# Kernel tuning notes

Measured on AMD Instinct MI355X. Metric: run time of the kernel, lower is better.

Reference implementation:

```python
import jax, jax.numpy as jnp
import numpy as np
import math

EMB_DIM = 1024
HEADS = 16
HEAD_DIM = EMB_DIM // HEADS
B, S = 2, 2048


def setup_inputs() -> dict:
    key = jax.random.key(0)
    k1, k2, k3, k4, k5 = jax.random.split(key, 5)
    X = jax.random.normal(k1, (B, S, EMB_DIM), dtype=jnp.float32)
    # causal mask: positions with 0.0 are masked to -inf (masked_fill(mask == 0.0, -inf))
    mask = jnp.tril(jnp.ones((S, S), dtype=jnp.float32))
    scale = 1.0 / math.sqrt(EMB_DIM)
    # torch Linear(emb_dim, 3*emb_dim): y = x @ W.T + b; store W pre-transposed [E, 3E]
    W_qkv = jax.random.normal(k2, (EMB_DIM, 3 * EMB_DIM), dtype=jnp.float32) * scale
    b_qkv = jnp.zeros((3 * EMB_DIM,), dtype=jnp.float32)
    W_o = jax.random.normal(k3, (EMB_DIM, EMB_DIM), dtype=jnp.float32) * scale
    b_o = jnp.zeros((EMB_DIM,), dtype=jnp.float32)
    return {"X": X, "mask": mask, "W_qkv": W_qkv, "b_qkv": b_qkv, "W_o": W_o, "b_o": b_o}


def reference(X, mask, W_qkv, b_qkv, W_o, b_o):
    # X: [B, S, E]
    Bn, Sn, E = X.shape
    qkv = X @ W_qkv + b_qkv                                   # [B, S, 3E]
    qkv = qkv.reshape(Bn, Sn, 3, HEADS, HEAD_DIM)
    qkv = jnp.transpose(qkv, (2, 0, 3, 1, 4))                  # [3, B, H, S, d]
    Q, K, V = qkv[0], qkv[1], qkv[2]
    inv_sqrt_d = 1.0 / math.sqrt(HEAD_DIM)
    scores = jnp.einsum('bhqd,bhkd->bhqk', Q, K) * inv_sqrt_d  # [B, H, S, S]
    scores = jnp.where(mask == 0.0, -jnp.inf, scores)
    attn = jax.nn.softmax(scores, axis=-1)
    # dropout omitted (eval mode / deterministic reference)
    out = jnp.einsum('bhqk,bhkd->bhqd', attn, V)               # [B, H, S, d]
    out = jnp.transpose(out, (0, 2, 1, 3)).reshape(Bn, Sn, E)
    return out @ W_o + b_o
```

## Files before the change

### kernel.cpp

```cpp
#include <hip/hip_runtime.h>
#include <hip/hip_bf16.h>
#include <cstdint>
#include <cstddef>

typedef __bf16 bf16_t;
typedef __attribute__((ext_vector_type(8))) __bf16 bf16x8;
typedef __attribute__((ext_vector_type(4))) __bf16 bf16x4;
typedef __attribute__((ext_vector_type(4))) float f32x4;

#define AS1 __attribute__((address_space(1)))
#define AS3 __attribute__((address_space(3)))

static constexpr int Bn = 2, Sn = 2048, En = 1024, Hn = 16, Dn = 64;

__device__ __forceinline__ uint32_t cvt_pk_bf16(float lo, float hi) {
  uint32_t r;
  asm("v_cvt_pk_bf16_f32 %0, %1, %2" : "=v"(r) : "v"(lo), "v"(hi));
  return r;
}

__global__ __launch_bounds__(256) void convert_f32_bf16(
    const float* __restrict__ in, bf16_t* __restrict__ out, int n) {
  int i = (blockIdx.x * 256 + threadIdx.x) * 4;
  if (i < n) {
    float4 v = *(const float4*)(in + i);
    bf16x4 o;
    o[0] = (bf16_t)v.x; o[1] = (bf16_t)v.y; o[2] = (bf16_t)v.z; o[3] = (bf16_t)v.w;
    *(bf16x4*)(out + i) = o;
  }
}

__global__ __launch_bounds__(256) void transpose_conv(
    const float* __restrict__ in, bf16_t* __restrict__ out, int R, int C) {
  __shared__ float tile[32][33];
  int bx = blockIdx.x * 32, by = blockIdx.y * 32;
  int tx = threadIdx.x & 31, ty = threadIdx.x >> 5;
#pragma unroll
  for (int i = 0; i < 32; i += 8)
    tile[ty + i][tx] = in[(size_t)(by + ty + i) * C + bx + tx];
  __syncthreads();
#pragma unroll
  for (int i = 0; i < 32; i += 8)
    out[(size_t)(bx + ty + i) * R + by + tx] = (bf16_t)tile[tx][ty + i];
}

__global__ __launch_bounds__(256) void transpose_v(
    const bf16_t* __restrict__ V, bf16_t* __restrict__ Vt) {
  __shared__ ushort tile[64][65];
  int bh = blockIdx.y, s0 = blockIdx.x * 64;
  int t = threadIdx.x;
  const ushort* src = (const ushort*)(V + ((size_t)bh * Sn + s0) * 64);
#pragma unroll
  for (int p = 0; p < 4; ++p) {
    int s = p * 16 + (t >> 4);
    int c = (t & 15) * 4;
    ushort4 v = *(const ushort4*)(src + (size_t)s * 64 + c);
    tile[s][c] = v.x; tile[s][c + 1] = v.y; tile[s][c + 2] = v.z; tile[s][c + 3] = v.w;
  }
  __syncthreads();
  ushort* dst = (ushort*)(Vt + ((size_t)bh * 64) * Sn + s0);
#pragma unroll
  for (int p = 0; p < 4; ++p) {
    int d = p * 16 + (t >> 4);
    int c = (t & 15) * 4;
    ushort4 v;
    v.x = tile[c][d]; v.y = tile[c + 1][d]; v.z = tile[c + 2][d]; v.w = tile[c + 3][d];
    *(ushort4*)(dst + (size_t)d * Sn + c) = v;
  }
}

template <int K_>
__device__ __forceinline__ void gemm_core(
    const bf16_t* __restrict__ A, const bf16_t* __restrict__ Bt,
    f32x4 (&acc)[4][4], int& col0, int& row0) {
  __shared__ bf16_t As[2][128 * 32];
  __shared__ bf16_t Bs[2][128 * 32];
  const int tid = threadIdx.x, lane = tid & 63, wid = tid >> 6;
  const int wm = wid >> 1, wn = wid & 1;
  const int m0 = blockIdx.y * 128, n0 = blockIdx.x * 128;
  const int KT = K_ / 32;

  auto stage = [&](bf16_t* as, bf16_t* bs, int kt) {
    int csw = ((lane & 3) ^ ((lane >> 2) & 3)) * 8;
#pragma unroll
    for (int j = 0; j < 2; ++j) {
      int r0 = wid * 32 + j * 16;
      const bf16_t* ga = A + (size_t)(m0 + r0 + (lane >> 2)) * K_ + kt * 32 + csw;
      __builtin_amdgcn_global_load_lds((const AS1 void*)ga, (AS3 void*)(as + r0 * 32), 16, 0, 0);
      const bf16_t* gb = Bt + (size_t)(n0 + r0 + (lane >> 2)) * K_ + kt * 32 + csw;
      __builtin_amdgcn_global_load_lds((const AS1 void*)gb, (AS3 void*)(bs + r0 * 32), 16, 0, 0);
    }
  };
  auto compute = [&](const bf16_t* as, const bf16_t* bs) {
    bf16x8 af[4], bfr[4];
    uint32_t swz = (uint32_t)(((lane >> 4) ^ (lane & 3)) << 4);
#pragma unroll
    for (int mi = 0; mi < 4; ++mi) {
      uint32_t row = (uint32_t)(wm * 64 + mi * 16 + (lane & 15));
      af[mi] = *(const bf16x8*)((const char*)as + row * 64 + swz);
    }
#pragma unroll
    for (int ni = 0; ni < 4; ++ni) {
      uint32_t row = (uint32_t)(wn * 64 + ni * 16 + (lane & 15));
      bfr[ni] = *(const bf16x8*)((const char*)bs + row * 64 + swz);
    }
#pragma unroll
    for (int mi = 0; mi < 4; ++mi)
#pragma unroll
      for (int ni = 0; ni < 4; ++ni)
        acc[mi][ni] = __builtin_amdgcn_mfma_f32_16x16x32_bf16(af[mi], bfr[ni], acc[mi][ni], 0, 0, 0);
  };

  stage(As[0], Bs[0], 0);
  __syncthreads();
  int cur = 0;
  for (int kt = 0; kt < KT - 1; ++kt) {
    stage(As[cur ^ 1], Bs[cur ^ 1], kt + 1);
    compute(As[cur], Bs[cur]);
    __syncthreads();
    cur ^= 1;
  }
  compute(As[cur], Bs[cur]);
  col0 = n0 + wn * 64 + (lane & 15);
  row0 = m0 + wm * 64 + ((lane >> 4) << 2);
}

__global__ __launch_bounds__(256) void gemm_qkv(
    const bf16_t* __restrict__ A, const bf16_t* __restrict__ Bt,
    const float* __restrict__ bias, bf16_t* __restrict__ Qb,
    bf16_t* __restrict__ Kb, bf16_t* __restrict__ Vb) {
  f32x4 acc[4][4] = {};
  int col0, row0;
  gemm_core<1024>(A, Bt, acc, col0, row0);
#pragma unroll
  for (int ni = 0; ni < 4; ++ni) {
    int n = col0 + ni * 16;
    float bv = bias[n];
    int which = n >> 10, nn = n & 1023;
    int h = nn >> 6, dd = nn & 63;
    bf16_t* dst = which == 0 ? Qb : (which == 1 ? Kb : Vb);
    float scl = which == 0 ? 0.125f * 1.44269504f : 1.0f;
#pragma unroll
    for (int mi = 0; mi < 4; ++mi)
#pragma unroll
      for (int i = 0; i < 4; ++i) {
        int m = row0 + mi * 16 + i;
        int b = m >> 11, s = m & 2047;
        float v = (acc[mi][ni][i] + bv) * scl;
        dst[(((size_t)b * Hn + h) * Sn + s) * 64 + dd] = (bf16_t)v;
      }
  }
}

__global__ __launch_bounds__(256) void gemm_out(
    const bf16_t* __restrict__ A, const bf16_t* __restrict__ Bt,
    const float* __restrict__ bias, float* __restrict__ out) {
  f32x4 acc[4][4] = {};
  int col0, row0;
  gemm_core<1024>(A, Bt, acc, col0, row0);
#pragma unroll
  for (int ni = 0; ni < 4; ++ni) {
    int n = col0 + ni * 16;
    float bv = bias[n];
#pragma unroll
    for (int mi = 0; mi < 4; ++mi)
#pragma unroll
      for (int i = 0; i < 4; ++i) {
        int m = row0 + mi * 16 + i;
        out[(size_t)m * En + n] = acc[mi][ni][i] + bv;
      }
  }
}

__global__ __launch_bounds__(256) void attn_fwd(
    const bf16_t* __restrict__ Qb, const bf16_t* __restrict__ Kb,
    const bf16_t* __restrict__ Vt, bf16_t* __restrict__ AO) {
  __shared__ bf16_t Ks[2][64 * 64];
  __shared__ bf16_t Vs[2][64 * 64];
  __shared__ bf16_t Ps[4][16 * 64];
  const int tid = threadIdx.x, lane = tid & 63, wid = tid >> 6;
  const int bh = blockIdx.x;
  const int pr = blockIdx.y;

  const int rl = lane >> 3;
  const int cp = lane & 7;
  auto issueKV = [&](int buf, int t) {
#pragma unroll
    for (int j = 0; j < 2; ++j) {
      int r = wid * 16 + j * 8 + rl;
      int sc = cp ^ rl;
      const bf16_t* gk = Kb + (((size_t)bh * Sn + t * 64 + r) << 6) + (sc << 3);
      __builtin_amdgcn_global_load_lds((const AS1 void*)gk,
          (AS3 void*)(&Ks[buf][wid * 1024 + j * 512]), 16, 0, 0);
      const bf16_t* gv = Vt + ((size_t)bh * 64 + r) * Sn + t * 64 + (sc << 3);
      __builtin_amdgcn_global_load_lds((const AS1 void*)gv,
          (AS3 void*)(&Vs[buf][wid * 1024 + j * 512]), 16, 0, 0);
    }
  };

  const int srcA = (((lane & 15) + ((lane & 16) << 1)) << 2);
  const int srcB = srcA + 64;
  const bool hi = lane >= 32;

  int buf = 0;
  issueKV(0, 0);

  for (int seg = 0; seg < 2; ++seg) {
    const int q_tile = seg ? 31 - pr : pr;
    const int ntseg = q_tile + 1;
    const int qb = q_tile * 64 + wid * 16;
    const int qmy = qb + (lane & 15);

    bf16x8 aq[2];
    {
      const bf16_t* qp = Qb + ((size_t)bh * Sn + qb + (lane & 15)) * 64 + ((lane >> 4) << 3);
      aq[0] = *(const bf16x8*)qp;
      aq[1] = *(const bf16x8*)(qp + 32);
    }
    f32x4 O[4] = {};
    float m_run = -1e30f, l_run = 0.f;

    for (int t = 0; t < ntseg; ++t) {
      asm volatile("s_waitcnt vmcnt(0)" ::: "memory");
      __syncthreads();
      if (t + 1 < ntseg) issueKV(buf ^ 1, t + 1);
      else if (seg == 0) issueKV(buf ^ 1, 0);
      const char* ksb = (const char*)Ks[buf];
      const char* vsb = (const char*)Vs[buf];
      f32x4 sc[4];
      __builtin_amdgcn_s_setprio(1);
#pragma unroll
      for (int ni = 0; ni < 4; ++ni) {
        int kvr = ni * 16 + (lane & 15);
        uint32_t o0 = (uint32_t)(kvr * 128 + ((lane >> 4) << 4)) ^ (uint32_t)((kvr & 7) << 4);
        uint32_t o1 = (uint32_t)(kvr * 128 + 64 + ((lane >> 4) << 4)) ^ (uint32_t)((kvr & 7) << 4);
        bf16x8 b0 = *(const bf16x8*)(ksb + o0);
        bf16x8 b1 = *(const bf16x8*)(ksb + o1);
        f32x4 z = {};
        z = __builtin_amdgcn_mfma_f32_16x16x32_bf16(b0, aq[0], z, 0, 0, 0);
        sc[ni] = __builtin_amdgcn_mfma_f32_16x16x32_bf16(b1, aq[1], z, 0, 0, 0);
      }
      __builtin_amdgcn_s_setprio(0);
      if (t == ntseg - 1) {
#pragma unroll
        for (int ni = 0; ni < 4; ++ni) {
          int kvbase = t * 64 + ni * 16 + ((lane >> 4) << 2);
#pragma unroll
          for (int i = 0; i < 4; ++i)
            if (kvbase + i > qmy) sc[ni][i] = -1e30f;
        }
      }
      float mt = sc[0][0];
#pragma unroll
      for (int ni = 0; ni < 4; ++ni)
#pragma unroll
        for (int i = 0; i < 4; ++i) mt = fmaxf(mt, sc[ni][i]);
      mt = fmaxf(mt, __shfl_xor(mt, 16));
      mt = fmaxf(mt, __shfl_xor(mt, 32));
      if (!__all(mt <= m_run + 11.5f)) {
        float mn = fmaxf(m_run, mt);
        float s = __builtin_exp2f(m_run - mn);
        m_run = mn;
        l_run *= s;
#pragma unroll
        for (int n2 = 0; n2 < 4; ++n2)
#pragma unroll
          for (int i = 0; i < 4; ++i) O[n2][i] *= s;
      }
      float rs = 0.f;
      uint32_t pk[4][2];
#pragma unroll
      for (int ni = 0; ni < 4; ++ni) {
        float p0 = __builtin_exp2f(sc[ni][0] - m_run);
        float p1 = __builtin_exp2f(sc[ni][1] - m_run);
        float p2 = __builtin_exp2f(sc[ni][2] - m_run);
        float p3 = __builtin_exp2f(sc[ni][3] - m_run);
        rs += (p0 + p1) + (p2 + p3);
        pk[ni][0] = cvt_pk_bf16(p0, p1);
        pk[ni][1] = cvt_pk_bf16(p2, p3);
      }
      rs += __shfl_xor(rs, 16);
      rs += __shfl_xor(rs, 32);
      l_run += rs;
      union U8 { uint32_t u[4]; bf16x8 v; } pw0, pw1;
#pragma unroll
      for (int w = 0; w < 4; ++w) {
        int srci = (w < 2) ? srcA : srcB;
        uint32_t x0 = (uint32_t)__builtin_amdgcn_ds_bpermute(srci, (int)pk[0][w & 1]);
        uint32_t y0 = (uint32_t)__builtin_amdgcn_ds_bpermute(srci, (int)pk[1][w & 1]);
        pw0.u[w] = hi ? y0 : x0;
        uint32_t x1 = (uint32_t)__builtin_amdgcn_ds_bpermute(srci, (int)pk[2][w & 1]);
        uint32_t y1 = (uint32_t)__builtin_amdgcn_ds_bpermute(srci, (int)pk[3][w & 1]);
        pw1.u[w] = hi ? y1 : x1;
      }
      __builtin_amdgcn_s_setprio(1);
#pragma unroll
      for (int n2 = 0; n2 < 4; ++n2) {
        int dr = n2 * 16 + (lane & 15);
        uint32_t o0 = (uint32_t)(dr * 128 + ((lane >> 4) << 4)) ^ (uint32_t)((dr & 7) << 4);
        uint32_t o1 = (uint32_t)(dr * 128 + 64 + ((lane >> 4) << 4)) ^ (uint32_t)((dr & 7) << 4);
        bf16x8 v0 = *(const bf16x8*)(vsb + o0);
        bf16x8 v1 = *(const bf16x8*)(vsb + o1);
        O[n2] = __builtin_amdgcn_mfma_f32_16x16x32_bf16(v0, pw0.v, O[n2], 0, 0, 0);
        O[n2] = __builtin_amdgcn_mfma_f32_16x16x32_bf16(v1, pw1.v, O[n2], 0, 0, 0);
      }
      __builtin_amdgcn_s_setprio(0);
      buf ^= 1;
    }
    char* pw = (char*)Ps[wid];
    const float inv = 1.0f / l_run;
    const int ql = lane & 15, g = lane >> 4;
#pragma unroll
    for (int n2 = 0; n2 < 4; ++n2)
#pragma unroll
      for (int p2 = 0; p2 < 2; ++p2) {
        uint32_t w = cvt_pk_bf16(O[n2][2 * p2] * inv, O[n2][2 * p2 + 1] * inv);
        uint32_t byte = (uint32_t)(ql * 128 + n2 * 32 + g * 8 + p2 * 4) ^ (uint32_t)((ql & 7) << 4);
        *(uint32_t*)(pw + byte) = w;
      }
    asm volatile("s_waitcnt lgkmcnt(0)" ::: "memory");
    __builtin_amdgcn_sched_barrier(0);
    int b = bh >> 4, h = bh & 15;
#pragma unroll
    for (int i = 0; i < 4; ++i) {
      int ql2 = (g << 2) + i;
      int qrow = qb + ql2;
#pragma unroll
      for (int n2 = 0; n2 < 4; ++n2) {
        int d = n2 * 16 + ql;
        uint32_t byte = (uint32_t)(ql2 * 128 + d * 2) ^ (uint32_t)((ql2 & 7) << 4);
        AO[((size_t)b * Sn + qrow) * En + h * 64 + d] = *(bf16_t*)(pw + byte);
      }
    }
  }
}

extern "C" void kernel_launch(void* const* d_in, const int* in_sizes, int n_in,
                              void* d_out, int out_size, void* d_ws, size_t ws_size,
                              hipStream_t stream) {
  const float* X     = (const float*)d_in[0];
  const float* W_qkv = (const float*)d_in[2];
  const float* b_qkv = (const float*)d_in[3];
  const float* W_o   = (const float*)d_in[4];
  const float* b_o   = (const float*)d_in[5];
  float* out = (float*)d_out;

  char* ws = (char*)d_ws;
  bf16_t* Xb  = (bf16_t*)(ws);
  bf16_t* WqT = (bf16_t*)(ws + 8388608);
  bf16_t* WoT = (bf16_t*)(ws + 14680064);
  bf16_t* Qb  = (bf16_t*)(ws + 16777216);
  bf16_t* Kb  = (bf16_t*)(ws + 25165824);
  bf16_t* Vb  = (bf16_t*)(ws + 33554432);
  bf16_t* Vt  = (bf16_t*)(ws + 41943040);
  bf16_t* AO  = (bf16_t*)(ws + 50331648);

  convert_f32_bf16<<<4096, 256, 0, stream>>>(X, Xb, Bn * Sn * En);
  transpose_conv<<<dim3(96, 32), 256, 0, stream>>>(W_qkv, WqT, 1024, 3072);
  transpose_conv<<<dim3(32, 32), 256, 0, stream>>>(W_o, WoT, 1024, 1024);
  gemm_qkv<<<dim3(24, 32), 256, 0, stream>>>(Xb, WqT, b_qkv, Qb, Kb, Vb);
  transpose_v<<<dim3(32, 32), 256, 0, stream>>>(Vb, Vt);
  attn_fwd<<<dim3(32, 16), 256, 0, stream>>>(Qb, Kb, Vt, AO);
  gemm_out<<<dim3(8, 32), 256, 0, stream>>>(AO, WoT, b_o, out);
}
```

Baseline: 224.4 us.

## Split attention blocks to one query tile each and halve out-GEMM M tile

The attention kernel drops the paired-query-tile scheme, where each block handled tiles pr and 31-pr in sequence, and launches one block per query tile (grid 32x32). Blocks are ordered so the heaviest causal tiles come first. The output projection GEMM is templated to a 64-row M tile, which doubles its block count from 256 to 512 so it fills the GPU better. In exchange, the attention blocks now carry uneven amounts of work and the Q/O setup and write-back cost is paid per block, while the GEMM reuses the B tile over fewer rows.

```diff
diff --git a/kernel.cpp b/kernel.cpp
--- a/kernel.cpp
+++ b/kernel.cpp
@@ -69,34 +69,39 @@
   }
 }
 
-template <int K_>
+template <int K_, int BM>
 __device__ __forceinline__ void gemm_core(
     const bf16_t* __restrict__ A, const bf16_t* __restrict__ Bt,
-    f32x4 (&acc)[4][4], int& col0, int& row0) {
-  __shared__ bf16_t As[2][128 * 32];
+    f32x4 (&acc)[BM / 32][4], int& col0, int& row0) {
+  __shared__ bf16_t As[2][BM * 32];
   __shared__ bf16_t Bs[2][128 * 32];
   const int tid = threadIdx.x, lane = tid & 63, wid = tid >> 6;
   const int wm = wid >> 1, wn = wid & 1;
-  const int m0 = blockIdx.y * 128, n0 = blockIdx.x * 128;
+  const int m0 = blockIdx.y * BM, n0 = blockIdx.x * 128;
   const int KT = K_ / 32;
+  constexpr int MI = BM / 32;
 
   auto stage = [&](bf16_t* as, bf16_t* bs, int kt) {
     int csw = ((lane & 3) ^ ((lane >> 2) & 3)) * 8;
 #pragma unroll
+    for (int j = 0; j < BM / 64; ++j) {
+      int r0 = wid * (BM / 4) + j * 16;
+      const bf16_t* ga = A + (size_t)(m0 + r0 + (lane >> 2)) * K_ + kt * 32 + csw;
+      __builtin_amdgcn_global_load_lds((const AS1 void*)ga, (AS3 void*)(as + r0 * 32), 16, 0, 0);
+    }
+#pragma unroll
     for (int j = 0; j < 2; ++j) {
       int r0 = wid * 32 + j * 16;
-      const bf16_t* ga = A + (size_t)(m0 + r0 + (lane >> 2)) * K_ + kt * 32 + csw;
-      __builtin_amdgcn_global_load_lds((const AS1 void*)ga, (AS3 void*)(as + r0 * 32), 16, 0, 0);
       const bf16_t* gb = Bt + (size_t)(n0 + r0 + (lane >> 2)) * K_ + kt * 32 + csw;
       __builtin_amdgcn_global_load_lds((const AS1 void*)gb, (AS3 void*)(bs + r0 * 32), 16, 0, 0);
     }
   };
   auto compute = [&](const bf16_t* as, const bf16_t* bs) {
-    bf16x8 af[4], bfr[4];
+    bf16x8 af[MI], bfr[4];
     uint32_t swz = (uint32_t)(((lane >> 4) ^ (lane & 3)) << 4);
 #pragma unroll
-    for (int mi = 0; mi < 4; ++mi) {
-      uint32_t row = (uint32_t)(wm * 64 + mi * 16 + (lane & 15));
+    for (int mi = 0; mi < MI; ++mi) {
+      uint32_t row = (uint32_t)(wm * (BM / 2) + mi * 16 + (lane & 15));
       af[mi] = *(const bf16x8*)((const char*)as + row * 64 + swz);
     }
 #pragma unroll
@@ -105,7 +110,7 @@
       bfr[ni] = *(const bf16x8*)((const char*)bs + row * 64 + swz);
     }
 #pragma unroll
-    for (int mi = 0; mi < 4; ++mi)
+    for (int mi = 0; mi < MI; ++mi)
 #pragma unroll
       for (int ni = 0; ni < 4; ++ni)
         acc[mi][ni] = __builtin_amdgcn_mfma_f32_16x16x32_bf16(af[mi], bfr[ni], acc[mi][ni], 0, 0, 0);
@@ -122,7 +127,7 @@
   }
   compute(As[cur], Bs[cur]);
   col0 = n0 + wn * 64 + (lane & 15);
-  row0 = m0 + wm * 64 + ((lane >> 4) << 2);
+  row0 = m0 + wm * (BM / 2) + ((lane >> 4) << 2);
 }
 
 __global__ __launch_bounds__(256) void gemm_qkv(
@@ -131,7 +136,7 @@
     bf16_t* __restrict__ Kb, bf16_t* __restrict__ Vb) {
   f32x4 acc[4][4] = {};
   int col0, row0;
-  gemm_core<1024>(A, Bt, acc, col0, row0);
+  gemm_core<1024, 128>(A, Bt, acc, col0, row0);
 #pragma unroll
   for (int ni = 0; ni < 4; ++ni) {
     int n = col0 + ni * 16;
@@ -155,15 +160,15 @@
 __global__ __launch_bounds__(256) void gemm_out(
     const bf16_t* __restrict__ A, const bf16_t* __restrict__ Bt,
     const float* __restrict__ bias, float* __restrict__ out) {
-  f32x4 acc[4][4] = {};
+  f32x4 acc[2][4] = {};
   int col0, row0;
-  gemm_core<1024>(A, Bt, acc, col0, row0);
+  gemm_core<1024, 64>(A, Bt, acc, col0, row0);
 #pragma unroll
   for (int ni = 0; ni < 4; ++ni) {
     int n = col0 + ni * 16;
     float bv = bias[n];
 #pragma unroll
-    for (int mi = 0; mi < 4; ++mi)
+    for (int mi = 0; mi < 2; ++mi)
 #pragma unroll
       for (int i = 0; i < 4; ++i) {
         int m = row0 + mi * 16 + i;
@@ -180,7 +185,11 @@
   __shared__ bf16_t Ps[4][16 * 64];
   const int tid = threadIdx.x, lane = tid & 63, wid = tid >> 6;
   const int bh = blockIdx.x;
-  const int pr = blockIdx.y;
+  const int y = blockIdx.y, gy = y & 7, ky = y >> 3;
+  const int q_tile = ky == 0 ? 31 - gy : (ky == 1 ? 16 + gy : (ky == 2 ? 15 - gy : gy));
+  const int nt = q_tile + 1;
+  const int qb = q_tile * 64 + wid * 16;
+  const int qmy = qb + (lane & 15);
 
   const int rl = lane >> 3;
   const int cp = lane & 7;
@@ -202,135 +211,127 @@
   const int srcB = srcA + 64;
   const bool hi = lane >= 32;
 
+  bf16x8 aq[2];
+  {
+    const bf16_t* qp = Qb + ((size_t)bh * Sn + qb + (lane & 15)) * 64 + ((lane >> 4) << 3);
+    aq[0] = *(const bf16x8*)qp;
+    aq[1] = *(const bf16x8*)(qp + 32);
+  }
+  f32x4 O[4] = {};
+  float m_run = -1e30f, l_run = 0.f;
+
   int buf = 0;
   issueKV(0, 0);
 
-  for (int seg = 0; seg < 2; ++seg) {
-    const int q_tile = seg ? 31 - pr : pr;
-    const int ntseg = q_tile + 1;
-    const int qb = q_tile * 64 + wid * 16;
-    const int qmy = qb + (lane & 15);
-
-    bf16x8 aq[2];
-    {
-      const bf16_t* qp = Qb + ((size_t)bh * Sn + qb + (lane & 15)) * 64 + ((lane >> 4) << 3);
-      aq[0] = *(const bf16x8*)qp;
-      aq[1] = *(const bf16x8*)(qp + 32);
-    }
-    f32x4 O[4] = {};
-    float m_run = -1e30f, l_run = 0.f;
-
-    for (int t = 0; t < ntseg; ++t) {
-      asm volatile("s_waitcnt vmcnt(0)" ::: "memory");
-      __syncthreads();
-      if (t + 1 < ntseg) issueKV(buf ^ 1, t + 1);
-      else if (seg == 0) issueKV(buf ^ 1, 0);
-      const char* ksb = (const char*)Ks[buf];
-      const char* vsb = (const char*)Vs[buf];
-      f32x4 sc[4];
-      __builtin_amdgcn_s_setprio(1);
+  for (int t = 0; t < nt; ++t) {
+    asm volatile("s_waitcnt vmcnt(0)" ::: "memory");
+    __syncthreads();
+    if (t + 1 < nt) issueKV(buf ^ 1, t + 1);
+    const char* ksb = (const char*)Ks[buf];
+    const char* vsb = (const char*)Vs[buf];
+    f32x4 sc[4];
+    __builtin_amdgcn_s_setprio(1);
+#pragma unroll
+    for (int ni = 0; ni < 4; ++ni) {
+      int kvr = ni * 16 + (lane & 15);
+      uint32_t o0 = (uint32_t)(kvr * 128 + ((lane >> 4) << 4)) ^ (uint32_t)((kvr & 7) << 4);
+      uint32_t o1 = (uint32_t)(kvr * 128 + 64 + ((lane >> 4) << 4)) ^ (uint32_t)((kvr & 7) << 4);
+      bf16x8 b0 = *(const bf16x8*)(ksb + o0);
+      bf16x8 b1 = *(const bf16x8*)(ksb + o1);
+      f32x4 z = {};
+      z = __builtin_amdgcn_mfma_f32_16x16x32_bf16(b0, aq[0], z, 0, 0, 0);
+      sc[ni] = __builtin_amdgcn_mfma_f32_16x16x32_bf16(b1, aq[1], z, 0, 0, 0);
+    }
+    __builtin_amdgcn_s_setprio(0);
+    if (t == nt - 1) {
 #pragma unroll
       for (int ni = 0; ni < 4; ++ni) {
-        int kvr = ni * 16 + (lane & 15);
-        uint32_t o0 = (uint32_t)(kvr * 128 + ((lane >> 4) << 4)) ^ (uint32_t)((kvr & 7) << 4);
-        uint32_t o1 = (uint32_t)(kvr * 128 + 64 + ((lane >> 4) << 4)) ^ (uint32_t)((kvr & 7) << 4);
-        bf16x8 b0 = *(const bf16x8*)(ksb + o0);
-        bf16x8 b1 = *(const bf16x8*)(ksb + o1);
-        f32x4 z = {};
-        z = __builtin_amdgcn_mfma_f32_16x16x32_bf16(b0, aq[0], z, 0, 0, 0);
-        sc[ni] = __builtin_amdgcn_mfma_f32_16x16x32_bf16(b1, aq[1], z, 0, 0, 0);
+        int kvbase = t * 64 + ni * 16 + ((lane >> 4) << 2);
+#pragma unroll
+        for (int i = 0; i < 4; ++i)
+          if (kvbase + i > qmy) sc[ni][i] = -1e30f;
       }
-      __builtin_amdgcn_s_setprio(0);
-      if (t == ntseg - 1) {
-#pragma unroll
-        for (int ni = 0; ni < 4; ++ni) {
-          int kvbase = t * 64 + ni * 16 + ((lane >> 4) << 2);
-#pragma unroll
-          for (int i = 0; i < 4; ++i)
-            if (kvbase + i > qmy) sc[ni][i] = -1e30f;
-        }
-      }
-      float mt = sc[0][0];
-#pragma unroll
-      for (int ni = 0; ni < 4; ++ni)
-#pragma unroll
-        for (int i = 0; i < 4; ++i) mt = fmaxf(mt, sc[ni][i]);
-      mt = fmaxf(mt, __shfl_xor(mt, 16));
-      mt = fmaxf(mt, __shfl_xor(mt, 32));
-      if (!__all(mt <= m_run + 11.5f)) {
-        float mn = fmaxf(m_run, mt);
-        float s = __builtin_exp2f(m_run - mn);
-        m_run = mn;
-        l_run *= s;
-#pragma unroll
-        for (int n2 = 0; n2 < 4; ++n2)
-#pragma unroll
-          for (int i = 0; i < 4; ++i) O[n2][i] *= s;
-      }
-      float rs = 0.f;
-      uint32_t pk[4][2];
-#pragma unroll
-      for (int ni = 0; ni < 4; ++ni) {
-        float p0 = __builtin_exp2f(sc[ni][0] - m_run);
-        float p1 = __builtin_exp2f(sc[ni][1] - m_run);
-        float p2 = __builtin_exp2f(sc[ni][2] - m_run);
-        float p3 = __builtin_exp2f(sc[ni][3] - m_run);
-        rs += (p0 + p1) + (p2 + p3);
-        pk[ni][0] = cvt_pk_bf16(p0, p1);
-        pk[ni][1] = cvt_pk_bf16(p2, p3);
-      }
-      rs += __shfl_xor(rs, 16);
-      rs += __shfl_xor(rs, 32);
-      l_run += rs;
-      union U8 { uint32_t u[4]; bf16x8 v; } pw0, pw1;
-#pragma unroll
-      for (int w = 0; w < 4; ++w) {
-        int srci = (w < 2) ? srcA : srcB;
-        uint32_t x0 = (uint32_t)__builtin_amdgcn_ds_bpermute(srci, (int)pk[0][w & 1]);
-        uint32_t y0 = (uint32_t)__builtin_amdgcn_ds_bpermute(srci, (int)pk[1][w & 1]);
-        pw0.u[w] = hi ? y0 : x0;
-        uint32_t x1 = (uint32_t)__builtin_amdgcn_ds_bpermute(srci, (int)pk[2][w & 1]);
-        uint32_t y1 = (uint32_t)__builtin_amdgcn_ds_bpermute(srci, (int)pk[3][w & 1]);
-        pw1.u[w] = hi ? y1 : x1;
-      }
-      __builtin_amdgcn_s_setprio(1);
-#pragma unroll
-      for (int n2 = 0; n2 < 4; ++n2) {
-        int dr = n2 * 16 + (lane & 15);
-        uint32_t o0 = (uint32_t)(dr * 128 + ((lane >> 4) << 4)) ^ (uint32_t)((dr & 7) << 4);
-        uint32_t o1 = (uint32_t)(dr * 128 + 64 + ((lane >> 4) << 4)) ^ (uint32_t)((dr & 7) << 4);
-        bf16x8 v0 = *(const bf16x8*)(vsb + o0);
-        bf16x8 v1 = *(const bf16x8*)(vsb + o1);
-        O[n2] = __builtin_amdgcn_mfma_f32_16x16x32_bf16(v0, pw0.v, O[n2], 0, 0, 0);
-        O[n2] = __builtin_amdgcn_mfma_f32_16x16x32_bf16(v1, pw1.v, O[n2], 0, 0, 0);
-      }
-      __builtin_amdgcn_s_setprio(0);
-      buf ^= 1;
-    }
-    char* pw = (char*)Ps[wid];
-    const float inv = 1.0f / l_run;
-    const int ql = lane & 15, g = lane >> 4;
-#pragma unroll
-    for (int n2 = 0; n2 < 4; ++n2)
-#pragma unroll
-      for (int p2 = 0; p2 < 2; ++p2) {
-        uint32_t w = cvt_pk_bf16(O[n2][2 * p2] * inv, O[n2][2 * p2 + 1] * inv);
-        uint32_t byte = (uint32_t)(ql * 128 + n2 * 32 + g * 8 + p2 * 4) ^ (uint32_t)((ql & 7) << 4);
-        *(uint32_t*)(pw + byte) = w;
-      }
-    asm volatile("s_waitcnt lgkmcnt(0)" ::: "memory");
-    __builtin_amdgcn_sched_barrier(0);
-    int b = bh >> 4, h = bh & 15;
-#pragma unroll
-    for (int i = 0; i < 4; ++i) {
-      int ql2 = (g << 2) + i;
-      int qrow = qb + ql2;
-#pragma unroll
-      for (int n2 = 0; n2 < 4; ++n2) {
-        int d = n2 * 16 + ql;
-        uint32_t byte = (uint32_t)(ql2 * 128 + d * 2) ^ (uint32_t)((ql2 & 7) << 4);
-        AO[((size_t)b * Sn + qrow) * En + h * 64 + d] = *(bf16_t*)(pw + byte);
-      }
+    }
+    float mt = sc[0][0];
+#pragma unroll
+    for (int ni = 0; ni < 4; ++ni)
+#pragma unroll
+      for (int i = 0; i < 4; ++i) mt = fmaxf(mt, sc[ni][i]);
+    mt = fmaxf(mt, __shfl_xor(mt, 16));
+    mt = fmaxf(mt, __shfl_xor(mt, 32));
+    if (!__all(mt <= m_run + 11.5f)) {
+      float mn = fmaxf(m_run, mt);
+      float s = __builtin_exp2f(m_run - mn);
+      m_run = mn;
+      l_run *= s;
+#pragma unroll
+      for (int n2 = 0; n2 < 4; ++n2)
+#pragma unroll
+        for (int i = 0; i < 4; ++i) O[n2][i] *= s;
+    }
+    float rs = 0.f;
+    uint32_t pk[4][2];
+#pragma unroll
+    for (int ni = 0; ni < 4; ++ni) {
+      float p0 = __builtin_exp2f(sc[ni][0] - m_run);
+      float p1 = __builtin_exp2f(sc[ni][1] - m_run);
+      float p2 = __builtin_exp2f(sc[ni][2] - m_run);
+      float p3 = __builtin_exp2f(sc[ni][3] - m_run);
+      rs += (p0 + p1) + (p2 + p3);
+      pk[ni][0] = cvt_pk_bf16(p0, p1);
+      pk[ni][1] = cvt_pk_bf16(p2, p3);
+    }
+    rs += __shfl_xor(rs, 16);
+    rs += __shfl_xor(rs, 32);
+    l_run += rs;
+    union U8 { uint32_t u[4]; bf16x8 v; } pw0, pw1;
+#pragma unroll
+    for (int w = 0; w < 4; ++w) {
+      int srci = (w < 2) ? srcA : srcB;
+      uint32_t x0 = (uint32_t)__builtin_amdgcn_ds_bpermute(srci, (int)pk[0][w & 1]);
+      uint32_t y0 = (uint32_t)__builtin_amdgcn_ds_bpermute(srci, (int)pk[1][w & 1]);
+      pw0.u[w] = hi ? y0 : x0;
+      uint32_t x1 = (uint32_t)__builtin_amdgcn_ds_bpermute(srci, (int)pk[2][w & 1]);
+      uint32_t y1 = (uint32_t)__builtin_amdgcn_ds_bpermute(srci, (int)pk[3][w & 1]);
+      pw1.u[w] = hi ? y1 : x1;
+    }
+    __builtin_amdgcn_s_setprio(1);
+#pragma unroll
+    for (int n2 = 0; n2 < 4; ++n2) {
+      int dr = n2 * 16 + (lane & 15);
+      uint32_t o0 = (uint32_t)(dr * 128 + ((lane >> 4) << 4)) ^ (uint32_t)((dr & 7) << 4);
+      uint32_t o1 = (uint32_t)(dr * 128 + 64 + ((lane >> 4) << 4)) ^ (uint32_t)((dr & 7) << 4);
+      bf16x8 v0 = *(const bf16x8*)(vsb + o0);
+      bf16x8 v1 = *(const bf16x8*)(vsb + o1);
+      O[n2] = __builtin_amdgcn_mfma_f32_16x16x32_bf16(v0, pw0.v, O[n2], 0, 0, 0);
+      O[n2] = __builtin_amdgcn_mfma_f32_16x16x32_bf16(v1, pw1.v, O[n2], 0, 0, 0);
+    }
+    __builtin_amdgcn_s_setprio(0);
+    buf ^= 1;
+  }
+  char* pw = (char*)Ps[wid];
+  const float inv = 1.0f / l_run;
+  const int ql = lane & 15, g = lane >> 4;
+#pragma unroll
+  for (int n2 = 0; n2 < 4; ++n2)
+#pragma unroll
+    for (int p2 = 0; p2 < 2; ++p2) {
+      uint32_t w = cvt_pk_bf16(O[n2][2 * p2] * inv, O[n2][2 * p2 + 1] * inv);
+      uint32_t byte = (uint32_t)(ql * 128 + n2 * 32 + g * 8 + p2 * 4) ^ (uint32_t)((ql & 7) << 4);
+      *(uint32_t*)(pw + byte) = w;
+    }
+  asm volatile("s_waitcnt lgkmcnt(0)" ::: "memory");
+  __builtin_amdgcn_sched_barrier(0);
+  int b = bh >> 4, h = bh & 15;
+#pragma unroll
+  for (int i = 0; i < 4; ++i) {
+    int ql2 = (g << 2) + i;
+    int qrow = qb + ql2;
+#pragma unroll
+    for (int n2 = 0; n2 < 4; ++n2) {
+      int d = n2 * 16 + ql;
+      uint32_t byte = (uint32_t)(ql2 * 128 + d * 2) ^ (uint32_t)((ql2 & 7) << 4);
+      AO[((size_t)b * Sn + qrow) * En + h * 64 + d] = *(bf16_t*)(pw + byte);
     }
   }
 }
@@ -360,6 +361,6 @@
   transpose_conv<<<dim3(32, 32), 256, 0, stream>>>(W_o, WoT, 1024, 1024);
   gemm_qkv<<<dim3(24, 32), 256, 0, stream>>>(Xb, WqT, b_qkv, Qb, Kb, Vb);
   transpose_v<<<dim3(32, 32), 256, 0, stream>>>(Vb, Vt);
-  attn_fwd<<<dim3(32, 16), 256, 0, stream>>>(Qb, Kb, Vt, AO);
-  gemm_out<<<dim3(8, 32), 256, 0, stream>>>(AO, WoT, b_o, out);
-}
+  attn_fwd<<<dim3(32, 32), 256, 0, stream>>>(Qb, Kb, Vt, AO);
+  gemm_out<<<dim3(8, 64), 256, 0, stream>>>(AO, WoT, b_o, out);
+}
```

Result: faster. 216.6 us (-3.5%).
